# Performance work log

Measured on AMD Instinct MI355X. Metric: run time of the kernel, lower is better.

## Reference

```python
import jax, jax.numpy as jnp
import numpy as np

N = 4096          # patch_dim**2, patch_dim=64
F_IN = 44         # pre_Nfeat = Nfeat/3
F_OUT = 44
K = 16            # min_nn - 8
RANK = 11         # rank_theta


def setup_inputs() -> dict:
    key = jax.random.key(0)
    ks = jax.random.split(key, 6)
    return {
        "h": jax.random.normal(ks[0], (1, N, F_IN), jnp.float32),
        "local_mask": jnp.ones((N, N), jnp.float32),
        "W_lab": jax.random.normal(ks[1], (F_IN, F_IN), jnp.float32) * (1.0 / np.sqrt(F_IN)),
        "b_lab": jax.random.normal(ks[2], (1, F_IN), jnp.float32) * 0.1,
        "W_th1": jax.random.normal(ks[3], (F_IN, F_IN * RANK), jnp.float32) * (1.0 / F_IN),
        "b_th1": jnp.zeros((1, RANK, F_IN), jnp.float32),
        "W_th2": jax.random.normal(ks[4], (F_IN, F_OUT * RANK), jnp.float32) * (1.0 / F_IN),
        "b_th2": jnp.zeros((1, RANK, F_OUT), jnp.float32),
        "W_thl": jax.random.normal(ks[5], (F_IN, RANK), jnp.float32) * (1.0 / np.sqrt(RANK)),
        "b_thl": jnp.zeros((1, RANK), jnp.float32),
    }


def reference(h, local_mask, W_lab, b_lab, W_th1, b_th1, W_th2, b_th2, W_thl, b_thl):
    # --- compute_graph: pairwise sq. distances, masked, self-dist forced minimal ---
    hh = h[0]                                        # [N, F]
    hg = jax.lax.stop_gradient(hh)                   # torch detaches h for the graph
    sq = jnp.sum(hg * hg, axis=-1)                   # [N]
    D = jnp.abs(sq[:, None] + sq[None, :] - 2.0 * (hg @ hg.T))
    D = D * local_mask - 2.0 * jnp.eye(N, dtype=D.dtype)
    # --- kNN: 25 smallest distances; keep ranks 9..24 as neighbors, rank 0 = self ---
    _, top_idx = jax.lax.top_k(-D, K + 9)            # [N, 25]
    nbr_idx = top_idx[:, 9:].reshape(-1)             # [N*K] node-major edge order
    ctr_idx = jnp.repeat(top_idx[:, 0], K)           # [N*K]
    # --- gather (irregular access, the kernel target) ---
    x_tilde1 = hh[nbr_idx]                           # [E, F] neighbor features
    x_tilde2 = hh[ctr_idx]                           # [E, F] center features
    labels = x_tilde1 - x_tilde2                     # [E, F]
    d_labels = jnp.sum(labels * labels, axis=-1).reshape(N, K)
    # --- edge-conditioned low-rank filter generation ---
    lab = jax.nn.leaky_relu(labels @ W_lab + b_lab, negative_slope=0.2)  # [E, F]
    theta1 = (lab @ W_th1).reshape(-1, RANK, F_IN) + b_th1               # [E, R, F]
    theta2 = (lab @ W_th2).reshape(-1, RANK, F_OUT) + b_th2              # [E, R, Fo]
    thetal = lab @ W_thl + b_thl                                         # [E, R]
    t = jnp.einsum('erf,ef->er', theta1, x_tilde1) * thetal              # [E, R]
    x = jnp.einsum('erf,er->ef', theta2, t)                              # [E, Fo]
    # --- distance-weighted mean over K neighbors (scatter-mean) ---
    x = x.reshape(N, K, F_OUT) * jnp.exp(-d_labels / 10.0)[:, :, None]
    x = jnp.mean(x, axis=1)
    return x.reshape(1, N, F_OUT)
```

## Files before the change

### kernel.cpp

```cpp
#include <hip/hip_runtime.h>
#include <float.h>

#define N 4096
#define FI 44
#define RK 11
#define KNN 16
#define NSEL 25
#define NROW 4
#define ME 496

typedef unsigned long long u64;
typedef unsigned int u32;

__global__ __launch_bounds__(256) void k_prep(const float* __restrict__ h,
                                              float* __restrict__ sq,
                                              float* __restrict__ hT,
                                              const float* __restrict__ W1,
                                              const float* __restrict__ b1,
                                              const float* __restrict__ W2,
                                              const float* __restrict__ b2,
                                              float* __restrict__ WrG,
                                              float* __restrict__ W2T4) {
  const int tid = threadIdx.x;
  if (blockIdx.x < 16) {
    int n = blockIdx.x * 256 + tid;
    const float4* hr = reinterpret_cast<const float4*>(h + (size_t)n * FI);
    float v[FI];
    float s = 0.f;
#pragma unroll
    for (int c4 = 0; c4 < 11; c4++) {
      float4 x = hr[c4];
      v[4*c4] = x.x; v[4*c4+1] = x.y; v[4*c4+2] = x.z; v[4*c4+3] = x.w;
      s += x.x*x.x + x.y*x.y + x.z*x.z + x.w*x.w;
    }
    sq[n] = s;
#pragma unroll
    for (int c = 0; c < FI; c++) hT[c * N + n] = v[c];
  } else {
    int idx0 = (blockIdx.x - 16) * 256 + tid;
    for (int idx = idx0; idx < 496 * FI; idx += 64 * 256) {
      int m = idx / FI, f = idx - m * FI;
      float v;
      if (m < 484)      { int c = m % FI, r = m / FI; v = W1[c * 484 + r * FI + f]; }
      else if (m < 495) { int r = m - 484; v = b1[r * FI + f]; }
      else v = 0.f;
      WrG[idx] = v;
    }
    for (int idx = idx0; idx < 496 * 64; idx += 64 * 256) {
      int mc = idx >> 8;
      int fo = (idx >> 2) & 63;
      int i  = idx & 3;
      int m  = 4 * mc + i;
      float v = 0.f;
      if (fo < FI && m < 495) {
        if (m < 484) { int c = m % FI, r = m / FI; v = W2[c * 484 + r * FI + fo]; }
        else         { v = b2[(m - 484) * FI + fo]; }
      }
      W2T4[idx] = v;
    }
  }
}

__global__ __launch_bounds__(512) void k_dist_topk(const float* __restrict__ hT,
                                                   const float* __restrict__ sq,
                                                   const float* __restrict__ mask,
                                                   int* __restrict__ ctr_idx,
                                                   int* __restrict__ nbr_idx) {
  __shared__ __align__(16) float hi[NROW][FI];
  __shared__ float sqi4[NROW];
  __shared__ u32 lmin[NROW][512];
  __shared__ u32 Tsh[NROW];
  __shared__ int cnts[NROW];
  __shared__ u64 cbuf[NROW][128];
  const int tid = threadIdx.x;
  const int r0 = blockIdx.x * NROW;

  if (tid < NROW) { cnts[tid] = 0; sqi4[tid] = sq[r0 + tid]; }
  for (int t = tid; t < NROW * FI; t += 512) {
    int rr = t / FI, c = t % FI;
    hi[rr][c] = hT[c * N + (r0 + rr)];
  }
  __syncthreads();

  const float4* sq4p = reinterpret_cast<const float4*>(sq);
  const float4* mask4 = reinterpret_cast<const float4*>(mask);
  float4 m4r[2][NROW];
  float4 sq4r[2];
#pragma unroll
  for (int s = 0; s < 2; s++) {
    sq4r[s] = sq4p[s * 512 + tid];
#pragma unroll
    for (int rr = 0; rr < NROW; rr++)
      m4r[s][rr] = mask4[(size_t)(r0 + rr) * 1024 + s * 512 + tid];
  }

  const float4* hT4 = reinterpret_cast<const float4*>(hT);
  float4 acc[NROW][2];
#pragma unroll
  for (int rr = 0; rr < NROW; rr++)
#pragma unroll
    for (int s = 0; s < 2; s++) acc[rr][s] = make_float4(0.f, 0.f, 0.f, 0.f);

#pragma unroll 4
  for (int c = 0; c < FI; c++) {
    float4 v0 = hT4[c * 1024 + tid];
    float4 v1 = hT4[c * 1024 + 512 + tid];
#pragma unroll
    for (int rr = 0; rr < NROW; rr++) {
      float hc = hi[rr][c];
      acc[rr][0].x += hc * v0.x; acc[rr][0].y += hc * v0.y;
      acc[rr][0].z += hc * v0.z; acc[rr][0].w += hc * v0.w;
      acc[rr][1].x += hc * v1.x; acc[rr][1].y += hc * v1.y;
      acc[rr][1].z += hc * v1.z; acc[rr][1].w += hc * v1.w;
    }
  }

  u32 key[NROW][8];
#pragma unroll
  for (int s = 0; s < 2; s++) {
    float4 sq4 = sq4r[s];
    int jb = s * 2048 + 4 * tid;
#pragma unroll
    for (int rr = 0; rr < NROW; rr++) {
      int row = r0 + rr;
      float4 m4 = m4r[s][rr];
      float sqr = sqi4[rr];
      float d0 = fabsf(sqr + sq4.x - 2.f * acc[rr][s].x) * m4.x;
      float d1 = fabsf(sqr + sq4.y - 2.f * acc[rr][s].y) * m4.y;
      float d2 = fabsf(sqr + sq4.z - 2.f * acc[rr][s].z) * m4.z;
      float d3 = fabsf(sqr + sq4.w - 2.f * acc[rr][s].w) * m4.w;
      d0 -= (jb + 0 == row) ? 2.f : 0.f;
      d1 -= (jb + 1 == row) ? 2.f : 0.f;
      d2 -= (jb + 2 == row) ? 2.f : 0.f;
      d3 -= (jb + 3 == row) ? 2.f : 0.f;
      u32 u0 = __float_as_uint(d0); u0 ^= (u32)((int)u0 >> 31) | 0x80000000u;
      u32 u1 = __float_as_uint(d1); u1 ^= (u32)((int)u1 >> 31) | 0x80000000u;
      u32 u2 = __float_as_uint(d2); u2 ^= (u32)((int)u2 >> 31) | 0x80000000u;
      u32 u3 = __float_as_uint(d3); u3 ^= (u32)((int)u3 >> 31) | 0x80000000u;
      key[rr][s * 4 + 0] = u0; key[rr][s * 4 + 1] = u1;
      key[rr][s * 4 + 2] = u2; key[rr][s * 4 + 3] = u3;
    }
  }

#pragma unroll
  for (int rr = 0; rr < NROW; rr++) {
    u32 m = key[rr][0];
#pragma unroll
    for (int i = 1; i < 8; i++) m = key[rr][i] < m ? key[rr][i] : m;
    lmin[rr][tid] = m;
  }
  __syncthreads();

  const int w = tid >> 6, lane = tid & 63;

  if (w < NROW) {
    u32 g = lmin[w][lane];
#pragma unroll
    for (int k = 1; k < 8; k++) {
      u32 x = lmin[w][64 * k + lane];
      g = x < g ? x : g;
    }
#pragma unroll
    for (int kk = 2; kk <= 64; kk <<= 1)
#pragma unroll
      for (int jj = kk >> 1; jj > 0; jj >>= 1) {
        u32 o = __shfl_xor(g, jj, 64);
        bool low = (lane & jj) == 0, asc = (lane & kk) == 0;
        u32 mn = o < g ? o : g, mx = o < g ? g : o;
        g = (low == asc) ? mn : mx;
      }
    if (lane == 24) Tsh[w] = g;
  }
  __syncthreads();

#pragma unroll
  for (int rr = 0; rr < NROW; rr++) {
    u32 Tr = Tsh[rr];
#pragma unroll
    for (int s = 0; s < 2; s++)
#pragma unroll
      for (int i = 0; i < 4; i++) {
        u32 kv = key[rr][s * 4 + i];
        if (kv <= Tr) {
          int p = atomicAdd(&cnts[rr], 1);
          if (p < 128) cbuf[rr][p] = ((u64)kv << 12) | (u64)(s * 2048 + 4 * tid + i);
        }
      }
  }
  __syncthreads();

  if (w < NROW) {
    const u64 UMAX = ~0ull;
    int cnt = cnts[w];
    u64 v0 = (lane < cnt) ? cbuf[w][lane] : UMAX;
    u64 v1 = (64 + lane < cnt) ? cbuf[w][64 + lane] : UMAX;
#pragma unroll
    for (int kk = 2; kk <= 128; kk <<= 1) {
#pragma unroll
      for (int jj = kk >> 1; jj > 0; jj >>= 1) {
        if (jj >= 64) {
          bool asc = (lane & kk) == 0;
          u64 mn = v0 < v1 ? v0 : v1, mx = v0 < v1 ? v1 : v0;
          v0 = asc ? mn : mx; v1 = asc ? mx : mn;
        } else {
          bool low = (lane & jj) == 0;
          bool asc0 = (lane & kk) == 0;
          bool asc1 = ((64 + lane) & kk) == 0;
          u64 o0 = __shfl_xor(v0, jj, 64);
          v0 = (low == asc0) ? (o0 < v0 ? o0 : v0) : (o0 < v0 ? v0 : o0);
          u64 o1 = __shfl_xor(v1, jj, 64);
          v1 = (low == asc1) ? (o1 < v1 ? o1 : v1) : (o1 < v1 ? v1 : o1);
        }
      }
    }
    int row = r0 + w;
    int idx = (int)(v0 & 4095ull);
    if (lane == 0) ctr_idx[row] = idx;
    if (lane >= 9 && lane < NSEL) nbr_idx[row * KNN + (lane - 9)] = idx;
  }
}

__global__ __launch_bounds__(256) void k_P1(const float* __restrict__ h,
                                            const float* __restrict__ WrG,
                                            float* __restrict__ P1e) {
  const int tid = threadIdx.x;
  const int grp = tid >> 6, lane = tid & 63;
  const int nb = blockIdx.x * 16 + grp * 4;
  const float4* h4 = reinterpret_cast<const float4*>(h);
  const float4* W4 = reinterpret_cast<const float4*>(WrG);

  float4 hq[4][11];
#pragma unroll
  for (int q = 0; q < 4; q++)
#pragma unroll
    for (int c4 = 0; c4 < 11; c4++)
      hq[q][c4] = h4[(size_t)(nb + q) * 11 + c4];

#pragma unroll
  for (int i = 0; i < 8; i++) {
    int m = lane + 64 * i;
    if (m < ME) {
      float a0 = 0.f, a1 = 0.f, a2 = 0.f, a3 = 0.f;
#pragma unroll
      for (int c4 = 0; c4 < 11; c4++) {
        float4 w = W4[m * 11 + c4];
        a0 += w.x*hq[0][c4].x + w.y*hq[0][c4].y + w.z*hq[0][c4].z + w.w*hq[0][c4].w;
        a1 += w.x*hq[1][c4].x + w.y*hq[1][c4].y + w.z*hq[1][c4].z + w.w*hq[1][c4].w;
        a2 += w.x*hq[2][c4].x + w.y*hq[2][c4].y + w.z*hq[2][c4].z + w.w*hq[2][c4].w;
        a3 += w.x*hq[3][c4].x + w.y*hq[3][c4].y + w.z*hq[3][c4].z + w.w*hq[3][c4].w;
      }
      P1e[(size_t)(nb + 0) * ME + m] = a0;
      P1e[(size_t)(nb + 1) * ME + m] = a1;
      P1e[(size_t)(nb + 2) * ME + m] = a2;
      P1e[(size_t)(nb + 3) * ME + m] = a3;
    }
  }
}

__global__ __launch_bounds__(256) void k_edge_out(
    const float* __restrict__ h,
    const int* __restrict__ ctr_idx, const int* __restrict__ nbr_idx,
    const float* __restrict__ W_lab, const float* __restrict__ b_lab,
    const float* __restrict__ Wl, const float* __restrict__ bl,
    const float* __restrict__ P1e,
    const float* __restrict__ W2T4,
    float* __restrict__ out)
{
  __shared__ __align__(16) float WlabT[FI][FI];
  __shared__ __align__(16) float lbl[64][FI];
  __shared__ __align__(16) float WlT[RK][FI];
  __shared__ __align__(16) float hcs[4][FI];
  __shared__ __align__(16) float GeL[4][ME];
  __shared__ __align__(16) float pacc[4][4][64];
  __shared__ float blabS[FI];
  __shared__ float blS[RK];
  __shared__ float tfs[64][12];
  __shared__ float wexpS[64];
  __shared__ int nbrL[64];
  __shared__ int ctrL[4];
  const int tid = threadIdx.x;
  const int b = blockIdx.x;
  const float4* h4 = reinterpret_cast<const float4*>(h);

  if (tid < 64) nbrL[tid] = nbr_idx[b * 64 + tid];
  if (tid < 4) ctrL[tid] = ctr_idx[b * 4 + tid];
  if (tid < RK) blS[tid] = bl[tid];
  if (tid >= 64 && tid < 64 + FI) blabS[tid - 64] = b_lab[tid - 64];
  for (int t = tid; t < FI * FI; t += 256) {
    int c = t / FI, f = t % FI;
    WlabT[f][c] = W_lab[t];
  }
  for (int t = tid; t < FI * RK; t += 256) {
    int c = t / RK, r = t % RK;
    WlT[r][c] = Wl[t];
  }
  __syncthreads();

  if (tid < 44) {
    int nn = tid / 11, c4 = tid % 11;
    *reinterpret_cast<float4*>(&hcs[nn][4 * c4]) = h4[(size_t)ctrL[nn] * 11 + c4];
  }
  __syncthreads();
  for (int t = tid; t < 64 * 11; t += 256) {
    int e = t / 11, c4 = t % 11;
    float4 hv = h4[(size_t)nbrL[e] * 11 + c4];
    float4 hc = *reinterpret_cast<const float4*>(&hcs[e >> 4][4 * c4]);
    float4 d;
    d.x = hv.x - hc.x; d.y = hv.y - hc.y; d.z = hv.z - hc.z; d.w = hv.w - hc.w;
    *reinterpret_cast<float4*>(&lbl[e][4 * c4]) = d;
  }
  __syncthreads();

  const int e = tid >> 2;
  const int g = tid & 3;

  float4 lbr[11];
#pragma unroll
  for (int c4 = 0; c4 < 11; c4++)
    lbr[c4] = *reinterpret_cast<const float4*>(&lbl[e][4 * c4]);
  if (g == 0) {
    float s = 0.f;
#pragma unroll
    for (int c4 = 0; c4 < 11; c4++)
      s += lbr[c4].x*lbr[c4].x + lbr[c4].y*lbr[c4].y + lbr[c4].z*lbr[c4].z + lbr[c4].w*lbr[c4].w;
    wexpS[e] = expf(-s * 0.1f) * (1.0f / 16.0f);
  }

  float la[11];
#pragma unroll
  for (int u = 0; u < 11; u++) {
    int f = g + 4 * u;
    float acc = blabS[f];
#pragma unroll
    for (int c4 = 0; c4 < 11; c4++) {
      float4 wv = *reinterpret_cast<const float4*>(&WlabT[f][4 * c4]);
      acc += wv.x*lbr[c4].x + wv.y*lbr[c4].y + wv.z*lbr[c4].z + wv.w*lbr[c4].w;
    }
    la[u] = acc >= 0.f ? acc : 0.2f * acc;
  }
  __syncthreads();
#pragma unroll
  for (int u = 0; u < 11; u++) lbl[e][g + 4 * u] = la[u];
  __syncthreads();

  {
#pragma unroll
    for (int c4 = 0; c4 < 11; c4++)
      lbr[c4] = *reinterpret_cast<const float4*>(&lbl[e][4 * c4]);
    const float* P1r = P1e + (size_t)nbrL[e] * ME;
    float wex = wexpS[e];
#pragma unroll
    for (int rr = 0; rr < 3; rr++) {
      int r = g + 4 * rr;
      if (r < RK) {
        float tp = 0.f, tlp = 0.f;
#pragma unroll
        for (int c4 = 0; c4 < 11; c4++) {
          float4 p4 = *reinterpret_cast<const float4*>(P1r + r * FI + 4 * c4);
          float4 w4 = *reinterpret_cast<const float4*>(&WlT[r][4 * c4]);
          float4 l4 = lbr[c4];
          tp  += l4.x*p4.x + l4.y*p4.y + l4.z*p4.z + l4.w*p4.w;
          tlp += l4.x*w4.x + l4.y*w4.y + l4.z*w4.z + l4.w*w4.w;
        }
        tfs[e][r] = (tp + P1r[484 + r]) * (tlp + blS[r]) * wex;
      }
    }
  }
  __syncthreads();

  const int nn = tid >> 6, lane = tid & 63;
  const int w = nn;
  if (lane < FI) {
    float acc2[RK];
#pragma unroll
    for (int r = 0; r < RK; r++) acc2[r] = 0.f;
    for (int k = 0; k < KNN; k++) {
      float lv = lbl[nn * 16 + k][lane];
#pragma unroll
      for (int r = 0; r < RK; r++) acc2[r] += lv * tfs[nn * 16 + k][r];
    }
#pragma unroll
    for (int r = 0; r < RK; r++) GeL[nn][r * FI + lane] = acc2[r];
  } else if (lane < FI + RK) {
    int r = lane - FI;
    float ss = 0.f;
    for (int k = 0; k < KNN; k++) ss += tfs[nn * 16 + k][r];
    GeL[nn][484 + r] = ss;
  } else if (lane == 55) {
    GeL[nn][495] = 0.f;
  }
  __syncthreads();

  {
    const float4* W2v = reinterpret_cast<const float4*>(W2T4);
    float a0 = 0.f, a1 = 0.f, a2 = 0.f, a3 = 0.f;
    for (int mc = w * 31; mc < (w + 1) * 31; mc++) {
      float4 wv = W2v[mc * 64 + lane];
      float4 g0 = *reinterpret_cast<const float4*>(&GeL[0][4 * mc]);
      float4 g1 = *reinterpret_cast<const float4*>(&GeL[1][4 * mc]);
      float4 g2 = *reinterpret_cast<const float4*>(&GeL[2][4 * mc]);
      float4 g3 = *reinterpret_cast<const float4*>(&GeL[3][4 * mc]);
      a0 += wv.x*g0.x + wv.y*g0.y + wv.z*g0.z + wv.w*g0.w;
      a1 += wv.x*g1.x + wv.y*g1.y + wv.z*g1.z + wv.w*g1.w;
      a2 += wv.x*g2.x + wv.y*g2.y + wv.z*g2.z + wv.w*g2.w;
      a3 += wv.x*g3.x + wv.y*g3.y + wv.z*g3.z + wv.w*g3.w;
    }
    pacc[w][0][lane] = a0;
    pacc[w][1][lane] = a1;
    pacc[w][2][lane] = a2;
    pacc[w][3][lane] = a3;
  }
  __syncthreads();

  if (tid < 4 * FI) {
    int n2 = tid / FI, fo = tid - (tid / FI) * FI;
    out[(size_t)(b * 4 + n2) * FI + fo] =
        pacc[0][n2][fo] + pacc[1][n2][fo] + pacc[2][n2][fo] + pacc[3][n2][fo];
  }
}

extern "C" void kernel_launch(void* const* d_in, const int* in_sizes, int n_in,
                              void* d_out, int out_size, void* d_ws, size_t ws_size,
                              hipStream_t stream) {
  const float* h     = (const float*)d_in[0];
  const float* mask  = (const float*)d_in[1];
  const float* W_lab = (const float*)d_in[2];
  const float* b_lab = (const float*)d_in[3];
  const float* W1    = (const float*)d_in[4];
  const float* b1    = (const float*)d_in[5];
  const float* W2    = (const float*)d_in[6];
  const float* b2    = (const float*)d_in[7];
  const float* Wl    = (const float*)d_in[8];
  const float* bl    = (const float*)d_in[9];

  float* sqw  = (float*)d_ws;
  float* hT   = sqw + N;
  int*   ctr  = (int*)(hT + (size_t)FI * N);
  int*   nbr  = ctr + N;
  float* P1e  = (float*)(nbr + N * KNN);
  float* WrG  = P1e + (size_t)N * ME;
  float* W2T4 = WrG + 496 * FI;

  k_prep<<<80, 256, 0, stream>>>(h, sqw, hT, W1, b1, W2, b2, WrG, W2T4);
  k_dist_topk<<<N / NROW, 512, 0, stream>>>(hT, sqw, mask, ctr, nbr);
  k_P1<<<N / 16, 256, 0, stream>>>(h, WrG, P1e);
  k_edge_out<<<N * KNN / 64, 256, 0, stream>>>(h, ctr, nbr, W_lab, b_lab, Wl, bl, P1e, W2T4, (float*)d_out);
}
```

Baseline: 96.01 us.

## Split distance top-k across column halves with global candidate merge; fuse P1 into prep

The fused distance/top-k kernel is split so that each row group is handled by two blocks, one per column half. Each block computes a local 25th-smallest threshold and appends its candidates to a per-row global buffer through an atomic counter. A new sort kernel then bitonic-sorts the merged candidates and selects the center and neighbor indices. Separately, the P1 projection is folded into the prep kernel, reading W1/b1 directly instead of going through a rearranged WrG copy, which saves one launch and one intermediate buffer. The aim is more blocks and lower register pressure in the distance sweep, at the cost of an extra memset, an extra kernel, global candidate traffic, and a 128-candidate cap shared by both halves.

```diff
diff --git a/kernel.cpp b/kernel.cpp
--- a/kernel.cpp
+++ b/kernel.cpp
@@ -12,15 +12,15 @@
 typedef unsigned long long u64;
 typedef unsigned int u32;
 
-__global__ __launch_bounds__(256) void k_prep(const float* __restrict__ h,
-                                              float* __restrict__ sq,
-                                              float* __restrict__ hT,
-                                              const float* __restrict__ W1,
-                                              const float* __restrict__ b1,
-                                              const float* __restrict__ W2,
-                                              const float* __restrict__ b2,
-                                              float* __restrict__ WrG,
-                                              float* __restrict__ W2T4) {
+__global__ __launch_bounds__(256) void k_prep_all(const float* __restrict__ h,
+                                                  float* __restrict__ sq,
+                                                  float* __restrict__ hT,
+                                                  const float* __restrict__ W1,
+                                                  const float* __restrict__ b1,
+                                                  const float* __restrict__ W2,
+                                                  const float* __restrict__ b2,
+                                                  float* __restrict__ P1e,
+                                                  float* __restrict__ W2T4) {
   const int tid = threadIdx.x;
   if (blockIdx.x < 16) {
     int n = blockIdx.x * 256 + tid;
@@ -36,17 +36,41 @@
     sq[n] = s;
 #pragma unroll
     for (int c = 0; c < FI; c++) hT[c * N + n] = v[c];
+  } else if (blockIdx.x < 272) {
+    const int grp = tid >> 6, lane = tid & 63;
+    const int nb = (blockIdx.x - 16) * 16 + grp * 4;
+    const float4* h4 = reinterpret_cast<const float4*>(h);
+    float4 hq[4][11];
+#pragma unroll
+    for (int q = 0; q < 4; q++)
+#pragma unroll
+      for (int c4 = 0; c4 < 11; c4++)
+        hq[q][c4] = h4[(size_t)(nb + q) * 11 + c4];
+#pragma unroll
+    for (int i = 0; i < 8; i++) {
+      int m = lane + 64 * i;
+      if (m < 495) {
+        const float4* wrow = reinterpret_cast<const float4*>(
+            (m < 484) ? W1 + (size_t)(m % FI) * 484 + (m / FI) * FI
+                      : b1 + (size_t)(m - 484) * FI);
+        float a0 = 0.f, a1 = 0.f, a2 = 0.f, a3 = 0.f;
+#pragma unroll
+        for (int c4 = 0; c4 < 11; c4++) {
+          float4 wv = wrow[c4];
+          a0 += wv.x*hq[0][c4].x + wv.y*hq[0][c4].y + wv.z*hq[0][c4].z + wv.w*hq[0][c4].w;
+          a1 += wv.x*hq[1][c4].x + wv.y*hq[1][c4].y + wv.z*hq[1][c4].z + wv.w*hq[1][c4].w;
+          a2 += wv.x*hq[2][c4].x + wv.y*hq[2][c4].y + wv.z*hq[2][c4].z + wv.w*hq[2][c4].w;
+          a3 += wv.x*hq[3][c4].x + wv.y*hq[3][c4].y + wv.z*hq[3][c4].z + wv.w*hq[3][c4].w;
+        }
+        P1e[(size_t)(nb + 0) * ME + m] = a0;
+        P1e[(size_t)(nb + 1) * ME + m] = a1;
+        P1e[(size_t)(nb + 2) * ME + m] = a2;
+        P1e[(size_t)(nb + 3) * ME + m] = a3;
+      }
+    }
   } else {
-    int idx0 = (blockIdx.x - 16) * 256 + tid;
-    for (int idx = idx0; idx < 496 * FI; idx += 64 * 256) {
-      int m = idx / FI, f = idx - m * FI;
-      float v;
-      if (m < 484)      { int c = m % FI, r = m / FI; v = W1[c * 484 + r * FI + f]; }
-      else if (m < 495) { int r = m - 484; v = b1[r * FI + f]; }
-      else v = 0.f;
-      WrG[idx] = v;
-    }
-    for (int idx = idx0; idx < 496 * 64; idx += 64 * 256) {
+    int idx0 = (blockIdx.x - 272) * 256 + tid;
+    for (int idx = idx0; idx < 496 * 64; idx += 16 * 256) {
       int mc = idx >> 8;
       int fo = (idx >> 2) & 63;
       int i  = idx & 3;
@@ -61,97 +85,83 @@
   }
 }
 
-__global__ __launch_bounds__(512) void k_dist_topk(const float* __restrict__ hT,
-                                                   const float* __restrict__ sq,
-                                                   const float* __restrict__ mask,
-                                                   int* __restrict__ ctr_idx,
-                                                   int* __restrict__ nbr_idx) {
+__global__ __launch_bounds__(512) void k_dist_sweep(const float* __restrict__ hT,
+                                                    const float* __restrict__ sq,
+                                                    const float* __restrict__ mask,
+                                                    int* __restrict__ gcnt,
+                                                    u64* __restrict__ gcand) {
   __shared__ __align__(16) float hi[NROW][FI];
-  __shared__ float sqi4[NROW];
+  __shared__ float sqi[NROW];
   __shared__ u32 lmin[NROW][512];
   __shared__ u32 Tsh[NROW];
   __shared__ int cnts[NROW];
   __shared__ u64 cbuf[NROW][128];
   const int tid = threadIdx.x;
-  const int r0 = blockIdx.x * NROW;
-
-  if (tid < NROW) { cnts[tid] = 0; sqi4[tid] = sq[r0 + tid]; }
+  const int rowgrp = blockIdx.x >> 1;
+  const int half = blockIdx.x & 1;
+  const int r0 = rowgrp * NROW;
+  const int w = tid >> 6, lane = tid & 63;
+  const int cb = half * 512 + tid;
+  const int jb = 4 * cb;
+
+  if (tid < NROW) { cnts[tid] = 0; sqi[tid] = sq[r0 + tid]; }
   for (int t = tid; t < NROW * FI; t += 512) {
     int rr = t / FI, c = t % FI;
     hi[rr][c] = hT[c * N + (r0 + rr)];
   }
   __syncthreads();
 
+  const float4* hT4 = reinterpret_cast<const float4*>(hT);
   const float4* sq4p = reinterpret_cast<const float4*>(sq);
   const float4* mask4 = reinterpret_cast<const float4*>(mask);
-  float4 m4r[2][NROW];
-  float4 sq4r[2];
-#pragma unroll
-  for (int s = 0; s < 2; s++) {
-    sq4r[s] = sq4p[s * 512 + tid];
-#pragma unroll
-    for (int rr = 0; rr < NROW; rr++)
-      m4r[s][rr] = mask4[(size_t)(r0 + rr) * 1024 + s * 512 + tid];
-  }
-
-  const float4* hT4 = reinterpret_cast<const float4*>(hT);
-  float4 acc[NROW][2];
+
+  float4 sq4 = sq4p[cb];
+  float4 m4r[NROW];
 #pragma unroll
   for (int rr = 0; rr < NROW; rr++)
-#pragma unroll
-    for (int s = 0; s < 2; s++) acc[rr][s] = make_float4(0.f, 0.f, 0.f, 0.f);
-
+    m4r[rr] = mask4[(size_t)(r0 + rr) * 1024 + cb];
+
+  float4 acc[NROW];
+#pragma unroll
+  for (int rr = 0; rr < NROW; rr++) acc[rr] = make_float4(0.f, 0.f, 0.f, 0.f);
 #pragma unroll 4
   for (int c = 0; c < FI; c++) {
-    float4 v0 = hT4[c * 1024 + tid];
-    float4 v1 = hT4[c * 1024 + 512 + tid];
+    float4 v = hT4[(size_t)c * 1024 + cb];
 #pragma unroll
     for (int rr = 0; rr < NROW; rr++) {
       float hc = hi[rr][c];
-      acc[rr][0].x += hc * v0.x; acc[rr][0].y += hc * v0.y;
-      acc[rr][0].z += hc * v0.z; acc[rr][0].w += hc * v0.w;
-      acc[rr][1].x += hc * v1.x; acc[rr][1].y += hc * v1.y;
-      acc[rr][1].z += hc * v1.z; acc[rr][1].w += hc * v1.w;
-    }
-  }
-
-  u32 key[NROW][8];
-#pragma unroll
-  for (int s = 0; s < 2; s++) {
-    float4 sq4 = sq4r[s];
-    int jb = s * 2048 + 4 * tid;
-#pragma unroll
-    for (int rr = 0; rr < NROW; rr++) {
-      int row = r0 + rr;
-      float4 m4 = m4r[s][rr];
-      float sqr = sqi4[rr];
-      float d0 = fabsf(sqr + sq4.x - 2.f * acc[rr][s].x) * m4.x;
-      float d1 = fabsf(sqr + sq4.y - 2.f * acc[rr][s].y) * m4.y;
-      float d2 = fabsf(sqr + sq4.z - 2.f * acc[rr][s].z) * m4.z;
-      float d3 = fabsf(sqr + sq4.w - 2.f * acc[rr][s].w) * m4.w;
-      d0 -= (jb + 0 == row) ? 2.f : 0.f;
-      d1 -= (jb + 1 == row) ? 2.f : 0.f;
-      d2 -= (jb + 2 == row) ? 2.f : 0.f;
-      d3 -= (jb + 3 == row) ? 2.f : 0.f;
-      u32 u0 = __float_as_uint(d0); u0 ^= (u32)((int)u0 >> 31) | 0x80000000u;
-      u32 u1 = __float_as_uint(d1); u1 ^= (u32)((int)u1 >> 31) | 0x80000000u;
-      u32 u2 = __float_as_uint(d2); u2 ^= (u32)((int)u2 >> 31) | 0x80000000u;
-      u32 u3 = __float_as_uint(d3); u3 ^= (u32)((int)u3 >> 31) | 0x80000000u;
-      key[rr][s * 4 + 0] = u0; key[rr][s * 4 + 1] = u1;
-      key[rr][s * 4 + 2] = u2; key[rr][s * 4 + 3] = u3;
-    }
-  }
-
+      acc[rr].x += hc * v.x; acc[rr].y += hc * v.y;
+      acc[rr].z += hc * v.z; acc[rr].w += hc * v.w;
+    }
+  }
+
+  u32 key[NROW][4];
 #pragma unroll
   for (int rr = 0; rr < NROW; rr++) {
-    u32 m = key[rr][0];
-#pragma unroll
-    for (int i = 1; i < 8; i++) m = key[rr][i] < m ? key[rr][i] : m;
-    lmin[rr][tid] = m;
-  }
-  __syncthreads();
-
-  const int w = tid >> 6, lane = tid & 63;
+    int row = r0 + rr;
+    float sqr = sqi[rr];
+    float d0 = fabsf(sqr + sq4.x - 2.f * acc[rr].x) * m4r[rr].x;
+    float d1 = fabsf(sqr + sq4.y - 2.f * acc[rr].y) * m4r[rr].y;
+    float d2 = fabsf(sqr + sq4.z - 2.f * acc[rr].z) * m4r[rr].z;
+    float d3 = fabsf(sqr + sq4.w - 2.f * acc[rr].w) * m4r[rr].w;
+    d0 -= (jb + 0 == row) ? 2.f : 0.f;
+    d1 -= (jb + 1 == row) ? 2.f : 0.f;
+    d2 -= (jb + 2 == row) ? 2.f : 0.f;
+    d3 -= (jb + 3 == row) ? 2.f : 0.f;
+    u32 u0 = __float_as_uint(d0); u0 ^= (u32)((int)u0 >> 31) | 0x80000000u;
+    u32 u1 = __float_as_uint(d1); u1 ^= (u32)((int)u1 >> 31) | 0x80000000u;
+    u32 u2 = __float_as_uint(d2); u2 ^= (u32)((int)u2 >> 31) | 0x80000000u;
+    u32 u3 = __float_as_uint(d3); u3 ^= (u32)((int)u3 >> 31) | 0x80000000u;
+    key[rr][0] = u0; key[rr][1] = u1; key[rr][2] = u2; key[rr][3] = u3;
+  }
+
+#pragma unroll
+  for (int rr = 0; rr < NROW; rr++) {
+    u32 m01 = key[rr][0] < key[rr][1] ? key[rr][0] : key[rr][1];
+    u32 m23 = key[rr][2] < key[rr][3] ? key[rr][2] : key[rr][3];
+    lmin[rr][tid] = m01 < m23 ? m01 : m23;
+  }
+  __syncthreads();
 
   if (w < NROW) {
     u32 g = lmin[w][lane];
@@ -177,84 +187,61 @@
   for (int rr = 0; rr < NROW; rr++) {
     u32 Tr = Tsh[rr];
 #pragma unroll
-    for (int s = 0; s < 2; s++)
-#pragma unroll
-      for (int i = 0; i < 4; i++) {
-        u32 kv = key[rr][s * 4 + i];
-        if (kv <= Tr) {
-          int p = atomicAdd(&cnts[rr], 1);
-          if (p < 128) cbuf[rr][p] = ((u64)kv << 12) | (u64)(s * 2048 + 4 * tid + i);
-        }
-      }
+    for (int i = 0; i < 4; i++) {
+      if (key[rr][i] <= Tr) {
+        int p = atomicAdd(&cnts[rr], 1);
+        if (p < 128) cbuf[rr][p] = ((u64)key[rr][i] << 12) | (u64)(jb + i);
+      }
+    }
   }
   __syncthreads();
 
   if (w < NROW) {
-    const u64 UMAX = ~0ull;
-    int cnt = cnts[w];
-    u64 v0 = (lane < cnt) ? cbuf[w][lane] : UMAX;
-    u64 v1 = (64 + lane < cnt) ? cbuf[w][64 + lane] : UMAX;
-#pragma unroll
-    for (int kk = 2; kk <= 128; kk <<= 1) {
-#pragma unroll
-      for (int jj = kk >> 1; jj > 0; jj >>= 1) {
-        if (jj >= 64) {
-          bool asc = (lane & kk) == 0;
-          u64 mn = v0 < v1 ? v0 : v1, mx = v0 < v1 ? v1 : v0;
-          v0 = asc ? mn : mx; v1 = asc ? mx : mn;
-        } else {
-          bool low = (lane & jj) == 0;
-          bool asc0 = (lane & kk) == 0;
-          bool asc1 = ((64 + lane) & kk) == 0;
-          u64 o0 = __shfl_xor(v0, jj, 64);
-          v0 = (low == asc0) ? (o0 < v0 ? o0 : v0) : (o0 < v0 ? v0 : o0);
-          u64 o1 = __shfl_xor(v1, jj, 64);
-          v1 = (low == asc1) ? (o1 < v1 ? o1 : v1) : (o1 < v1 ? v1 : o1);
-        }
-      }
-    }
     int row = r0 + w;
-    int idx = (int)(v0 & 4095ull);
-    if (lane == 0) ctr_idx[row] = idx;
-    if (lane >= 9 && lane < NSEL) nbr_idx[row * KNN + (lane - 9)] = idx;
+    int cw = cnts[w]; if (cw > 128) cw = 128;
+    int base = 0;
+    if (lane == 0) base = atomicAdd(&gcnt[row], cw);
+    base = __shfl(base, 0, 64);
+    for (int i = lane; i < cw; i += 64) {
+      int dst = base + i;
+      if (dst < 128) gcand[(size_t)row * 128 + dst] = cbuf[w][i];
+    }
   }
 }
 
-__global__ __launch_bounds__(256) void k_P1(const float* __restrict__ h,
-                                            const float* __restrict__ WrG,
-                                            float* __restrict__ P1e) {
+__global__ __launch_bounds__(512) void k_sort(const int* __restrict__ gcnt,
+                                              const u64* __restrict__ gcand,
+                                              int* __restrict__ ctr_idx,
+                                              int* __restrict__ nbr_idx) {
   const int tid = threadIdx.x;
-  const int grp = tid >> 6, lane = tid & 63;
-  const int nb = blockIdx.x * 16 + grp * 4;
-  const float4* h4 = reinterpret_cast<const float4*>(h);
-  const float4* W4 = reinterpret_cast<const float4*>(WrG);
-
-  float4 hq[4][11];
-#pragma unroll
-  for (int q = 0; q < 4; q++)
-#pragma unroll
-    for (int c4 = 0; c4 < 11; c4++)
-      hq[q][c4] = h4[(size_t)(nb + q) * 11 + c4];
-
-#pragma unroll
-  for (int i = 0; i < 8; i++) {
-    int m = lane + 64 * i;
-    if (m < ME) {
-      float a0 = 0.f, a1 = 0.f, a2 = 0.f, a3 = 0.f;
-#pragma unroll
-      for (int c4 = 0; c4 < 11; c4++) {
-        float4 w = W4[m * 11 + c4];
-        a0 += w.x*hq[0][c4].x + w.y*hq[0][c4].y + w.z*hq[0][c4].z + w.w*hq[0][c4].w;
-        a1 += w.x*hq[1][c4].x + w.y*hq[1][c4].y + w.z*hq[1][c4].z + w.w*hq[1][c4].w;
-        a2 += w.x*hq[2][c4].x + w.y*hq[2][c4].y + w.z*hq[2][c4].z + w.w*hq[2][c4].w;
-        a3 += w.x*hq[3][c4].x + w.y*hq[3][c4].y + w.z*hq[3][c4].z + w.w*hq[3][c4].w;
-      }
-      P1e[(size_t)(nb + 0) * ME + m] = a0;
-      P1e[(size_t)(nb + 1) * ME + m] = a1;
-      P1e[(size_t)(nb + 2) * ME + m] = a2;
-      P1e[(size_t)(nb + 3) * ME + m] = a3;
-    }
-  }
+  const int w = tid >> 6, lane = tid & 63;
+  const int row = blockIdx.x * 8 + w;
+  int cnt = gcnt[row]; if (cnt > 128) cnt = 128;
+  const u64 UMAX = ~0ull;
+  u64 v0 = (lane < cnt) ? gcand[(size_t)row * 128 + lane] : UMAX;
+  u64 v1 = (64 + lane < cnt) ? gcand[(size_t)row * 128 + 64 + lane] : UMAX;
+#pragma unroll
+  for (int kk = 2; kk <= 128; kk <<= 1) {
+#pragma unroll
+    for (int jj = kk >> 1; jj > 0; jj >>= 1) {
+      if (jj >= 64) {
+        bool asc = (lane & kk) == 0;
+        u64 mn = v0 < v1 ? v0 : v1, mx = v0 < v1 ? v1 : v0;
+        v0 = asc ? mn : mx; v1 = asc ? mx : mn;
+      } else {
+        bool low = (lane & jj) == 0;
+        bool asc0 = (lane & kk) == 0;
+        bool asc1 = ((64 + lane) & kk) == 0;
+        u64 o0 = __shfl_xor(v0, jj, 64);
+        v0 = (low == asc0) ? (o0 < v0 ? o0 : v0) : (o0 < v0 ? v0 : o0);
+        u64 o1 = __shfl_xor(v1, jj, 64);
+        v1 = (low == asc1) ? (o1 < v1 ? o1 : v1) : (o1 < v1 ? v1 : o1);
+      }
+    }
+  }
+  int idx = (int)(v0 & 4095ull);
+  if (lane == 0) ctr_idx[row] = idx;
+  if (lane >= 9 && lane < NSEL) nbr_idx[row * KNN + (lane - 9)] = idx;
 }
 
 __global__ __launch_bounds__(256) void k_edge_out(
@@ -433,16 +420,18 @@
   const float* Wl    = (const float*)d_in[8];
   const float* bl    = (const float*)d_in[9];
 
-  float* sqw  = (float*)d_ws;
-  float* hT   = sqw + N;
-  int*   ctr  = (int*)(hT + (size_t)FI * N);
-  int*   nbr  = ctr + N;
-  float* P1e  = (float*)(nbr + N * KNN);
-  float* WrG  = P1e + (size_t)N * ME;
-  float* W2T4 = WrG + 496 * FI;
-
-  k_prep<<<80, 256, 0, stream>>>(h, sqw, hT, W1, b1, W2, b2, WrG, W2T4);
-  k_dist_topk<<<N / NROW, 512, 0, stream>>>(hT, sqw, mask, ctr, nbr);
-  k_P1<<<N / 16, 256, 0, stream>>>(h, WrG, P1e);
+  u64*   gcand = (u64*)d_ws;
+  int*   gcnt  = (int*)(gcand + (size_t)N * 128);
+  float* sqw   = (float*)(gcnt + N);
+  float* hT    = sqw + N;
+  int*   ctr   = (int*)(hT + (size_t)FI * N);
+  int*   nbr   = ctr + N;
+  float* P1e   = (float*)(nbr + N * KNN);
+  float* W2T4  = P1e + (size_t)N * ME;
+
+  hipMemsetAsync(gcnt, 0, N * sizeof(int), stream);
+  k_prep_all<<<288, 256, 0, stream>>>(h, sqw, hT, W1, b1, W2, b2, P1e, W2T4);
+  k_dist_sweep<<<2 * (N / NROW), 512, 0, stream>>>(hT, sqw, mask, gcnt, gcand);
+  k_sort<<<N / 8, 512, 0, stream>>>(gcnt, gcand, ctr, nbr);
   k_edge_out<<<N * KNN / 64, 256, 0, stream>>>(h, ctr, nbr, W_lab, b_lab, Wl, bl, P1e, W2T4, (float*)d_out);
 }
```

New measurement: 105.2 us. 1.1x slower.
